# Kernel tuning notes

Hardware: AMD Instinct MI355X
Metric: run time of the kernel (lower is better)

Reference implementation:

```python
import jax, jax.numpy as jnp
import numpy as np

V, D, L, H, T, B = 128, 256, 2, 4, 4096, 8
DK, DV = 128, 256           # key_dim=0.5*D, value_dim=1.0*D (fla GLA defaults)
HK, HV = DK // H, DV // H   # 32, 64
GLN = 16.0                  # gate_logit_normalizer
CH = 64                     # chunk size
EPS = 1e-5

def layernorm(x, w, b):
    mu = x.mean(-1, keepdims=True)
    var = ((x - mu) ** 2).mean(-1, keepdims=True)
    return (x - mu) * jax.lax.rsqrt(var + EPS) * w + b

def gla_chunk(q, k, v, gk, scale):
    # q,k,gk: [B,T,H,HK], v: [B,T,H,HV]; gk are per-key log decay gates (<=0)
    B_, T_, H_, dk = q.shape
    dv = v.shape[-1]
    N = T_ // CH
    def rs(x):
        d = x.shape[-1]
        return x.reshape(B_, N, CH, H_, d).transpose(0, 3, 1, 2, 4)  # [B,H,N,C,d]
    q, k, v, gk = rs(q), rs(k), rs(v), rs(gk)
    b = jnp.cumsum(gk, axis=3)                       # inclusive within-chunk cumlog decay
    q_s = q * jnp.exp(b) * scale
    k_i = k * jnp.exp(-b)                            # for intra-chunk attention
    k_e = k * jnp.exp(b[..., -1:, :] - b)            # decayed to chunk end, for state update
    mask = jnp.tril(jnp.ones((CH, CH), bool))
    att = jnp.einsum('bhncd,bhnmd->bhncm', q_s, k_i)
    att = jnp.where(mask, att, 0.0)
    o_intra = jnp.einsum('bhncm,bhnmd->bhncd', att, v)
    g_last = jnp.exp(b[..., -1, :])                  # [B,H,N,dk] full-chunk decay
    kv = jnp.einsum('bhncd,bhnce->bhnde', k_e, v)    # [B,H,N,dk,dv]
    def step(S, inp):
        qc, gl, kvc = inp
        o = jnp.einsum('bhcd,bhde->bhce', qc, S)
        return S * gl[..., None] + kvc, o
    S0 = jnp.zeros((B_, H_, dk, dv), q.dtype)
    xs = (jnp.moveaxis(q_s, 2, 0), jnp.moveaxis(g_last, 2, 0), jnp.moveaxis(kv, 2, 0))
    _, o_inter = jax.lax.scan(step, S0, xs)
    o = o_intra + jnp.moveaxis(o_inter, 0, 2)        # [B,H,N,C,dv]
    return o.transpose(0, 2, 3, 1, 4).reshape(B_, T_, H_, dv)

def gla_attn(x, wq, wk, wv, wg, gk_w1, gk_w2, gk_b2, gnorm_w, wo):
    B_, T_, _ = x.shape
    q = (x @ wq).reshape(B_, T_, H, HK)
    k = (x @ wk).reshape(B_, T_, H, HK)
    v = (x @ wv).reshape(B_, T_, H, HV)
    gk = jax.nn.log_sigmoid(x @ gk_w1 @ gk_w2 + gk_b2) / GLN
    gk = gk.reshape(B_, T_, H, HK)
    o = gla_chunk(q, k, v, gk, HK ** -0.5)           # [B,T,H,HV]
    g = (x @ wg).reshape(B_, T_, H, HV)
    rms = jax.lax.rsqrt((o * o).mean(-1, keepdims=True) + EPS)
    o = o * rms * gnorm_w * (g * jax.nn.sigmoid(g))  # FusedRMSNormSwishGate
    return o.reshape(B_, T_, DV) @ wo

def setup_inputs() -> dict:
    key = jax.random.key(0)
    ks = jax.random.split(key, 16)
    s = 0.02
    return {
        'tokens': jax.random.randint(ks[0], (B, T), 0, V),
        'embed': jax.random.normal(ks[1], (V, D)) * s,
        'ln_w': jnp.ones((L, D)), 'ln_b': jnp.zeros((L, D)),
        'wq': jax.random.normal(ks[2], (L, D, DK)) * s,
        'wk': jax.random.normal(ks[3], (L, D, DK)) * s,
        'wv': jax.random.normal(ks[4], (L, D, DV)) * s,
        'wg': jax.random.normal(ks[5], (L, D, DV)) * s,
        'gk_w1': jax.random.normal(ks[6], (L, D, 16)) * s,
        'gk_w2': jax.random.normal(ks[7], (L, 16, DK)) * s,
        'gk_b2': jnp.zeros((L, DK)),
        'gnorm_w': jnp.ones((L, HV)),
        'wo': jax.random.normal(ks[8], (L, DV, D)) * s,
        'mlp_w1': jax.random.normal(ks[9], (L, D, 2 * D)) * s,
        'mlp_b1': jnp.zeros((L, 2 * D)),
        'mlp_w2': jax.random.normal(ks[10], (L, 2 * D, D)) * s,
        'mlp_b2': jnp.zeros((L, D)),
        'head_w': jax.random.normal(ks[11], (D, V)) * s,
        'head_b': jnp.zeros((V,)),
    }

def reference(tokens, embed, ln_w, ln_b, wq, wk, wv, wg, gk_w1, gk_w2, gk_b2,
              gnorm_w, wo, mlp_w1, mlp_b1, mlp_w2, mlp_b2, head_w, head_b):
    x = embed[tokens]
    for i in range(L):
        h = layernorm(x, ln_w[i], ln_b[i])
        x = x + gla_attn(h, wq[i], wk[i], wv[i], wg[i], gk_w1[i], gk_w2[i],
                         gk_b2[i], gnorm_w[i], wo[i])
        h = layernorm(x, ln_w[i], ln_b[i])
        x = x + jax.nn.gelu(h @ mlp_w1[i] + mlp_b1[i], approximate=False) @ mlp_w2[i] + mlp_b2[i]
    return x @ head_w + head_b
```

## Files before the change

kernel.cpp:

```cpp
#include <hip/hip_runtime.h>
#include <hip/hip_bf16.h>
#include <math.h>

namespace {

constexpr int Bq = 8, Tq = 4096, Dq = 256, Lq = 2, Hq = 4;
constexpr int DKq = 128, DVq = 256, HKq = 32, HVq = 64;
constexpr int Nq = Tq / 64;
constexpr int Mq = Bq * Tq;
constexpr int SQ = 896;
constexpr float SCALEq = 0.17677669529663688f;
constexpr int WL = 1114112;

typedef __hip_bfloat16 bf16;
typedef __attribute__((ext_vector_type(8))) short bf16x8;
typedef __attribute__((ext_vector_type(4))) float f32x4;

__device__ __forceinline__ float b2f(bf16 x) { return __bfloat162float(x); }

__device__ __forceinline__ bf16x8 ld8(const bf16* p) { return *(const bf16x8*)p; }
__device__ __forceinline__ bf16x8 ld8(const float* p) {
  const float4* q4 = (const float4*)p;
  float4 a = q4[0], b = q4[1];
  float v[8] = {a.x, a.y, a.z, a.w, b.x, b.y, b.z, b.w};
  bf16x8 r;
#pragma unroll
  for (int i = 0; i < 8; i++) r[i] = __builtin_bit_cast(short, __float2bfloat16(v[i]));
  return r;
}

__device__ __forceinline__ void wsplit2(float v, bf16* hi, bf16* lo) {
  bf16 h = __float2bfloat16(v);
  *hi = h; *lo = __float2bfloat16(v - b2f(h));
}

__global__ void k_wprep(const float* __restrict__ wq, const float* __restrict__ wk,
                        const float* __restrict__ wv, const float* __restrict__ wg,
                        const float* __restrict__ g1, const float* __restrict__ g2,
                        const float* __restrict__ wo, const float* __restrict__ m1,
                        const float* __restrict__ m2, const float* __restrict__ hw,
                        bf16* __restrict__ Wt) {
  int g = blockIdx.x * 256 + threadIdx.x;
  if (g >= 2 * 540672 + 32768) return;
  if (g < 2 * 540672) {
    int l = g / 540672, r = g % 540672;
    bf16* dst = Wt + (size_t)l * WL;
    if (r < 196608) {
      int k, nf; float v;
      if (r < 32768)       { int r2 = r;          k = r2 >> 7; nf = (r2 & 127);       v = wq[l*32768 + r2]; }
      else if (r < 65536)  { int r2 = r - 32768;  k = r2 >> 7; nf = 128 + (r2 & 127); v = wk[l*32768 + r2]; }
      else if (r < 131072) { int r2 = r - 65536;  k = r2 >> 8; nf = 256 + (r2 & 255); v = wv[l*65536 + r2]; }
      else                 { int r2 = r - 131072; k = r2 >> 8; nf = 512 + (r2 & 255); v = wg[l*65536 + r2]; }
      wsplit2(v, &dst[(size_t)nf*256 + k], &dst[229376 + (size_t)nf*256 + k]);
    } else if (r < 212992) {
      int r2 = r - 196608; int k = r2 >> 7, n = r2 & 127;
      float v = 0.f;
#pragma unroll
      for (int i = 0; i < 16; i++) v += g1[l*4096 + k*16 + i] * g2[l*2048 + i*128 + n];
      int nf = 768 + n;
      wsplit2(v, &dst[(size_t)nf*256 + k], &dst[229376 + (size_t)nf*256 + k]);
    } else if (r < 278528) {
      int r2 = r - 212992; int k = r2 >> 8, n = r2 & 255;
      wsplit2(wo[l*65536 + r2], &dst[458752 + (size_t)n*256 + k], &dst[524288 + (size_t)n*256 + k]);
    } else if (r < 409600) {
      int r2 = r - 278528; int k = r2 >> 9, n = r2 & 511;
      wsplit2(m1[l*131072 + r2], &dst[589824 + (size_t)n*256 + k], &dst[720896 + (size_t)n*256 + k]);
    } else {
      int r2 = r - 409600; int k = r2 >> 8, n = r2 & 255;
      wsplit2(m2[l*131072 + r2], &dst[851968 + (size_t)n*512 + k], &dst[983040 + (size_t)n*512 + k]);
    }
  } else {
    int r2 = g - 2 * 540672; int k = r2 >> 7, n = r2 & 127;
    wsplit2(hw[r2], &Wt[2228224 + (size_t)n*256 + k], &Wt[2228224 + 32768 + (size_t)n*256 + k]);
  }
}

__global__ void k_embed(const int* __restrict__ tok, const float* __restrict__ emb,
                        float* __restrict__ x) {
  int row = blockIdx.x, i = threadIdx.x;
  x[(size_t)row * Dq + i] = emb[(size_t)tok[row] * Dq + i];
}

__global__ void k_ln(const float* __restrict__ x, const float* __restrict__ w,
                     const float* __restrict__ bb, bf16* __restrict__ h) {
  int row = blockIdx.x, i = threadIdx.x;
  float v = x[(size_t)row * Dq + i];
  float s = v, s2 = v * v;
#pragma unroll
  for (int o = 32; o > 0; o >>= 1) { s += __shfl_down(s, o, 64); s2 += __shfl_down(s2, o, 64); }
  __shared__ float rs[4], rs2[4];
  if ((i & 63) == 0) { rs[i >> 6] = s; rs2[i >> 6] = s2; }
  __syncthreads();
  float sum = rs[0] + rs[1] + rs[2] + rs[3];
  float sum2 = rs2[0] + rs2[1] + rs2[2] + rs2[3];
  float mu = sum * (1.f / Dq);
  float var = fmaxf(sum2 * (1.f / Dq) - mu * mu, 0.f);
  float r = rsqrtf(var + 1e-5f);
  h[(size_t)row * Dq + i] = __float2bfloat16((v - mu) * r * w[i] + bb[i]);
}

template <typename AT, typename OT, int EPI, bool BIAS, bool ACC>
__global__ __launch_bounds__(256) void k_mgemm(const AT* __restrict__ A,
                                               const bf16* __restrict__ Wt,
                                               const float* __restrict__ bias,
                                               OT* __restrict__ C, int K, int N) {
  __shared__ __attribute__((aligned(16))) bf16 At[128 * 72];
  __shared__ __attribute__((aligned(16))) bf16 Bh[128 * 72];
  __shared__ __attribute__((aligned(16))) bf16 Bl[128 * 72];
  const bf16* Whi = Wt;
  const bf16* Wlo = Wt + (size_t)K * N;
  int tid = threadIdx.x;
  int row0 = blockIdx.x * 128, col0 = blockIdx.y * 128;
  int lane = tid & 63, wave = tid >> 6;
  int wm = (wave >> 1) * 64, wn = (wave & 1) * 64;
  int lr = lane & 15, lk = (lane >> 4) * 8;
  f32x4 acc[4][4];
#pragma unroll
  for (int m = 0; m < 4; m++)
#pragma unroll
    for (int n = 0; n < 4; n++) acc[m][n] = (f32x4){0.f, 0.f, 0.f, 0.f};

  for (int k0 = 0; k0 < K; k0 += 64) {
#pragma unroll
    for (int p = 0; p < 4; p++) {
      int cix = p * 256 + tid, r = cix >> 3, j = (cix & 7) * 8;
      *(bf16x8*)&At[r * 72 + j] = ld8(A + (size_t)(row0 + r) * K + k0 + j);
    }
#pragma unroll
    for (int p = 0; p < 4; p++) {
      int cix = p * 256 + tid, r = cix >> 3, j = (cix & 7) * 8;
      size_t go = (size_t)(col0 + r) * K + k0 + j;
      *(bf16x8*)&Bh[r * 72 + j] = *(const bf16x8*)(Whi + go);
      *(bf16x8*)&Bl[r * 72 + j] = *(const bf16x8*)(Wlo + go);
    }
    __syncthreads();
#pragma unroll
    for (int kk = 0; kk < 64; kk += 32) {
      bf16x8 af[4], bhf[4], blf[4];
#pragma unroll
      for (int m = 0; m < 4; m++) af[m] = *(bf16x8*)&At[(wm + m * 16 + lr) * 72 + kk + lk];
#pragma unroll
      for (int n = 0; n < 4; n++) {
        bhf[n] = *(bf16x8*)&Bh[(wn + n * 16 + lr) * 72 + kk + lk];
        blf[n] = *(bf16x8*)&Bl[(wn + n * 16 + lr) * 72 + kk + lk];
      }
#pragma unroll
      for (int m = 0; m < 4; m++)
#pragma unroll
        for (int n = 0; n < 4; n++) {
          acc[m][n] = __builtin_amdgcn_mfma_f32_16x16x32_bf16(af[m], bhf[n], acc[m][n], 0, 0, 0);
          acc[m][n] = __builtin_amdgcn_mfma_f32_16x16x32_bf16(af[m], blf[n], acc[m][n], 0, 0, 0);
        }
    }
    __syncthreads();
  }
#pragma unroll
  for (int m = 0; m < 4; m++) {
#pragma unroll
    for (int n = 0; n < 4; n++) {
      int col = col0 + wn + n * 16 + lr;
      int rowb = row0 + wm + m * 16 + (lane >> 4) * 4;
      float bv = BIAS ? bias[col] : 0.f;
#pragma unroll
      for (int j = 0; j < 4; j++) {
        float v = acc[m][n][j] + bv;
        if (EPI == 2) v = 0.5f * v * (1.f + erff(v * 0.70710678118654752f));
        if (EPI == 3 && col >= 768) {
          float t = v + bias[col - 768];
          v = (fminf(t, 0.f) - log1pf(expf(-fabsf(t)))) * (1.f / 16.f);
        }
        size_t oi = (size_t)(rowb + j) * N + col;
        if constexpr (ACC) C[oi] += v;
        else if constexpr (sizeof(OT) == 2) C[oi] = __float2bfloat16(v);
        else C[oi] = v;
      }
    }
  }
}

__global__ __launch_bounds__(256) void k_intra(bf16* QKVG,
                                               bf16* __restrict__ O,
                                               bf16* __restrict__ KVt,
                                               float* __restrict__ GL) {
  int blk = blockIdx.x;
  int n = blk & 63, h = (blk >> 6) & 3, b = blk >> 8;
  __shared__ __attribute__((aligned(16))) char smem[47488];
  float* bshT = (float*)smem;
  bf16*  kvS  = (bf16*)smem;
  float* glv  = (float*)(smem + 8448);
  bf16*  vT   = (bf16*)(smem + 8576);
  bf16*  kiAH = (bf16*)(smem + 17792);
  bf16*  kiAL = (bf16*)(smem + 22400);
  bf16*  qsH  = (bf16*)(smem + 27008);
  bf16*  qsL  = (bf16*)(smem + 32128);
  bf16*  kiBH = (bf16*)(smem + 37248);
  bf16*  kiBL = (bf16*)(smem + 42368);
  bf16*  aH   = (bf16*)(smem + 27008);
  bf16*  aL   = (bf16*)(smem + 36224);
  int tid = threadIdx.x;
  int lane = tid & 63, wave = tid >> 6;
  int lr = lane & 15, lg = lane >> 4;
  size_t tbase = (size_t)b * Tq + n * 64;
  int bh = b * Hq + h;

  {
    int c = tid >> 2, dc = (tid & 3) * 8;
    bf16x8 g8 = *(const bf16x8*)(QKVG + (tbase + c) * SQ + 768 + h * HKq + dc);
#pragma unroll
    for (int i = 0; i < 8; i++) bshT[(dc + i) * 66 + c] = b2f(__builtin_bit_cast(bf16, (short)g8[i]));
  }
  __syncthreads();
#pragma unroll
  for (int dd = 0; dd < 8; dd++) {
    int d = wave * 8 + dd;
    float v = bshT[d * 66 + lane];
#pragma unroll
    for (int o = 1; o < 64; o <<= 1) {
      float t = __shfl_up(v, (unsigned)o, 64);
      if (lane >= o) v += t;
    }
    bshT[d * 66 + lane] = v;
  }
  __syncthreads();
  if (tid < 32) {
    float g = expf(bshT[tid * 66 + 63]);
    glv[tid] = g;
    GL[(size_t)(bh * Nq + n) * 32 + tid] = g;
  }
  {
    int c = tid >> 2, dc = (tid & 3) * 8;
    size_t qoff = (tbase + c) * SQ + h * HKq + dc;
    bf16x8 q8 = *(const bf16x8*)(QKVG + qoff);
    bf16x8 k8 = *(const bf16x8*)(QKVG + qoff + 128);
    bf16x8 qh8, ql8, kh8, kl8;
#pragma unroll
    for (int i = 0; i < 8; i++) {
      float bv = bshT[(dc + i) * 66 + c];
      float qv = b2f(__builtin_bit_cast(bf16, (short)q8[i])) * expf(bv) * SCALEq;
      float kv = b2f(__builtin_bit_cast(bf16, (short)k8[i])) * expf(-bv);
      bf16 qh = __float2bfloat16(qv); bf16 ql = __float2bfloat16(qv - b2f(qh));
      bf16 kh = __float2bfloat16(kv); bf16 kl = __float2bfloat16(kv - b2f(kh));
      qh8[i] = __builtin_bit_cast(short, qh); ql8[i] = __builtin_bit_cast(short, ql);
      kh8[i] = __builtin_bit_cast(short, kh); kl8[i] = __builtin_bit_cast(short, kl);
      kiAH[(dc + i) * 72 + c] = kh; kiAL[(dc + i) * 72 + c] = kl;
    }
    *(bf16x8*)&qsH[c * 40 + dc] = qh8;
    *(bf16x8*)&qsL[c * 40 + dc] = ql8;
    *(bf16x8*)&kiBH[c * 40 + dc] = kh8;
    *(bf16x8*)&kiBL[c * 40 + dc] = kl8;
    *(bf16x8*)(QKVG + qoff) = qh8;
  }
#pragma unroll
  for (int p = 0; p < 2; p++) {
    int idx = p * 256 + tid;
    int c = idx & 63, ec = (idx >> 6) * 8;
    bf16x8 v8 = *(const bf16x8*)(QKVG + (tbase + c) * SQ + 256 + h * HVq + ec);
#pragma unroll
    for (int i = 0; i < 8; i++) vT[(ec + i) * 72 + c] = __builtin_bit_cast(bf16, (short)v8[i]);
  }
  __syncthreads();
  f32x4 accq[4];
#pragma unroll
  for (int t = 0; t < 4; t++) accq[t] = (f32x4){0.f, 0.f, 0.f, 0.f};
  {
    bf16x8 afh = *(bf16x8*)&qsH[(wave * 16 + lr) * 40 + lg * 8];
    bf16x8 afl = *(bf16x8*)&qsL[(wave * 16 + lr) * 40 + lg * 8];
#pragma unroll
    for (int t = 0; t < 4; t++) {
      bf16x8 bh = *(bf16x8*)&kiBH[(t * 16 + lr) * 40 + lg * 8];
      bf16x8 bl = *(bf16x8*)&kiBL[(t * 16 + lr) * 40 + lg * 8];
      accq[t] = __builtin_amdgcn_mfma_f32_16x16x32_bf16(afh, bh, accq[t], 0, 0, 0);
      accq[t] = __builtin_amdgcn_mfma_f32_16x16x32_bf16(afh, bl, accq[t], 0, 0, 0);
      accq[t] = __builtin_amdgcn_mfma_f32_16x16x32_bf16(afl, bh, accq[t], 0, 0, 0);
    }
  }
  __syncthreads();
#pragma unroll
  for (int t = 0; t < 4; t++)
#pragma unroll
    for (int j = 0; j < 4; j++) {
      int row = wave * 16 + lg * 4 + j;
      int col = t * 16 + lr;
      float v = (col <= row) ? accq[t][j] : 0.f;
      bf16 hi = __float2bfloat16(v);
      aH[row * 72 + col] = hi;
      aL[row * 72 + col] = __float2bfloat16(v - b2f(hi));
    }
  __syncthreads();
  f32x4 acco[4];
#pragma unroll
  for (int t = 0; t < 4; t++) acco[t] = (f32x4){0.f, 0.f, 0.f, 0.f};
#pragma unroll
  for (int ks = 0; ks < 2; ks++) {
    bf16x8 ah = *(bf16x8*)&aH[(wave * 16 + lr) * 72 + ks * 32 + lg * 8];
    bf16x8 al = *(bf16x8*)&aL[(wave * 16 + lr) * 72 + ks * 32 + lg * 8];
#pragma unroll
    for (int t = 0; t < 4; t++) {
      bf16x8 bfv = *(bf16x8*)&vT[(t * 16 + lr) * 72 + ks * 32 + lg * 8];
      acco[t] = __builtin_amdgcn_mfma_f32_16x16x32_bf16(ah, bfv, acco[t], 0, 0, 0);
      acco[t] = __builtin_amdgcn_mfma_f32_16x16x32_bf16(al, bfv, acco[t], 0, 0, 0);
    }
  }
#pragma unroll
  for (int t = 0; t < 4; t++)
#pragma unroll
    for (int j = 0; j < 4; j++) {
      int row = wave * 16 + lg * 4 + j, e = t * 16 + lr;
      O[(tbase + row) * DVq + h * HVq + e] = __float2bfloat16(acco[t][j]);
    }
  f32x4 acck[2];
  acck[0] = (f32x4){0.f, 0.f, 0.f, 0.f};
  acck[1] = (f32x4){0.f, 0.f, 0.f, 0.f};
#pragma unroll
  for (int ks = 0; ks < 2; ks++) {
    bf16x8 akh = *(bf16x8*)&kiAH[((wave >> 1) * 16 + lr) * 72 + ks * 32 + lg * 8];
    bf16x8 akl = *(bf16x8*)&kiAL[((wave >> 1) * 16 + lr) * 72 + ks * 32 + lg * 8];
#pragma unroll
    for (int t = 0; t < 2; t++) {
      bf16x8 bfv = *(bf16x8*)&vT[(((wave & 1) * 2 + t) * 16 + lr) * 72 + ks * 32 + lg * 8];
      acck[t] = __builtin_amdgcn_mfma_f32_16x16x32_bf16(akh, bfv, acck[t], 0, 0, 0);
      acck[t] = __builtin_amdgcn_mfma_f32_16x16x32_bf16(akl, bfv, acck[t], 0, 0, 0);
    }
  }
#pragma unroll
  for (int t = 0; t < 2; t++)
#pragma unroll
    for (int j = 0; j < 4; j++) {
      int d = (wave >> 1) * 16 + lg * 4 + j;
      int e = ((wave & 1) * 2 + t) * 16 + lr;
      kvS[d * 72 + e] = __float2bfloat16(acck[t][j] * glv[d]);
    }
  __syncthreads();
  size_t kbase = (size_t)(bh * Nq + n) * 2048;
  {
    int d = tid >> 3, cc = (tid & 7) * 8;
    *(bf16x8*)&KVt[kbase + d * 64 + cc] = *(bf16x8*)&kvS[d * 72 + cc];
  }
}

__global__ __launch_bounds__(256) void k_inter(const bf16* __restrict__ QKVG,
                                               const float* __restrict__ GL,
                                               const bf16* __restrict__ KVt,
                                               bf16* __restrict__ O) {
  int blk = blockIdx.x;
  int es = blk & 7, h = (blk >> 3) & 3, b = blk >> 5;
  int e0 = es * 8;
  __shared__ __attribute__((aligned(16))) bf16 kvl[64 * 32 * 8];
  __shared__ float gl[64 * 32];
  __shared__ float S[64 * 32 * 8];
  int tid = threadIdx.x;
  int bh = b * Hq + h;
  const float* glp = GL + (size_t)bh * Nq * 32;
#pragma unroll
  for (int p = 0; p < 8; p++) { int i = p * 256 + tid; gl[i] = glp[i]; }
  const bf16* kvp = KVt + (size_t)bh * Nq * 2048 + e0;
#pragma unroll
  for (int p = 0; p < 8; p++) {
    int c8 = p * 256 + tid;
    *(bf16x8*)&kvl[c8 * 8] = *(const bf16x8*)(kvp + (size_t)(c8 >> 5) * 2048 + (size_t)(c8 & 31) * 64);
  }
  __syncthreads();
  {
    int pe = tid & 7, pd = tid >> 3;
    float s = 0.f;
    for (int n = 0; n < 64; n++) {
      S[(n * 32 + pd) * 8 + pe] = s;
      s = s * gl[n * 32 + pd] + b2f(kvl[(n * 32 + pd) * 8 + pe]);
    }
  }
  __syncthreads();
  int c = tid >> 2, ep = tid & 3;
  for (int n = 0; n < 64; n++) {
    size_t tbase = (size_t)b * Tq + n * 64;
    const bf16* qp = QKVG + (tbase + c) * SQ + h * HKq;
    const float* Sp = &S[n * 256];
    float a0 = 0.f, a1 = 0.f;
#pragma unroll
    for (int j = 0; j < 4; j++) {
      bf16x8 q8 = *(const bf16x8*)(qp + j * 8);
#pragma unroll
      for (int i = 0; i < 8; i++) {
        float qf = b2f(__builtin_bit_cast(bf16, (short)q8[i]));
        int d = j * 8 + i;
        a0 += qf * Sp[d * 8 + ep];
        a1 += qf * Sp[d * 8 + ep + 4];
      }
    }
    size_t oi = (tbase + c) * DVq + h * HVq + e0 + ep;
    O[oi] = __float2bfloat16(b2f(O[oi]) + a0);
    O[oi + 4] = __float2bfloat16(b2f(O[oi + 4]) + a1);
  }
}

__global__ void k_gate(bf16* __restrict__ O, const bf16* __restrict__ QKVG,
                       const float* __restrict__ gnw) {
  int row = blockIdx.x, tid = threadIdx.x;
  int e = tid & 63;
  float o = b2f(O[(size_t)row * DVq + tid]);
  float s = o * o;
#pragma unroll
  for (int of = 32; of > 0; of >>= 1) s += __shfl_xor(s, of, 64);
  float r = rsqrtf(s * (1.f / 64.f) + 1e-5f);
  float g = b2f(QKVG[(size_t)row * SQ + 512 + tid]);
  float sw = g / (1.f + expf(-g));
  O[(size_t)row * DVq + tid] = __float2bfloat16(o * r * gnw[e] * sw);
}

}

extern "C" void kernel_launch(void* const* d_in, const int* in_sizes, int n_in,
                              void* d_out, int out_size, void* d_ws, size_t ws_size,
                              hipStream_t stream) {
  const int*   tok  = (const int*)d_in[0];
  const float* emb  = (const float*)d_in[1];
  const float* ln_w = (const float*)d_in[2];
  const float* ln_b = (const float*)d_in[3];
  const float* wq   = (const float*)d_in[4];
  const float* wk   = (const float*)d_in[5];
  const float* wv   = (const float*)d_in[6];
  const float* wg   = (const float*)d_in[7];
  const float* gkw1 = (const float*)d_in[8];
  const float* gkw2 = (const float*)d_in[9];
  const float* gkb2 = (const float*)d_in[10];
  const float* gnw  = (const float*)d_in[11];
  const float* wo   = (const float*)d_in[12];
  const float* mw1  = (const float*)d_in[13];
  const float* mb1  = (const float*)d_in[14];
  const float* mw2  = (const float*)d_in[15];
  const float* mb2  = (const float*)d_in[16];
  const float* hw   = (const float*)d_in[17];
  const float* hb   = (const float*)d_in[18];

  if (ws_size < 134217728u) return;
  char* w = (char*)d_ws;
  float* X    = (float*)w;
  bf16*  Ob   = (bf16*)(w + 33554432);
  bf16*  Hbf  = Ob;
  bf16*  QKVG = (bf16*)(w + 50331648);
  bf16*  KVt  = (bf16*)(w + 109051904);
  float* GLb  = (float*)(w + 117440512);
  bf16*  Wt   = (bf16*)(w + 117702656);
  bf16*  MLPH = QKVG;

  dim3 blk(256);
  k_wprep<<<4353, blk, 0, stream>>>(wq, wk, wv, wg, gkw1, gkw2, wo, mw1, mw2, hw, Wt);
  k_embed<<<Mq, blk, 0, stream>>>(tok, emb, X);

  for (int l = 0; l < Lq; l++) {
    const bf16* Wl = Wt + (size_t)l * WL;
    k_ln<<<Mq, blk, 0, stream>>>(X, ln_w + l * Dq, ln_b + l * Dq, Hbf);
    k_mgemm<bf16, bf16, 3, false, false><<<dim3(256, 7), blk, 0, stream>>>(Hbf, Wl, gkb2 + l * DKq, QKVG, 256, SQ);
    k_intra<<<Bq * Hq * Nq, blk, 0, stream>>>(QKVG, Ob, KVt, GLb);
    k_inter<<<Bq * Hq * 8, blk, 0, stream>>>(QKVG, GLb, KVt, Ob);
    k_gate<<<Mq, blk, 0, stream>>>(Ob, QKVG, gnw + l * HVq);
    k_mgemm<bf16, float, 0, false, true><<<dim3(256, 2), blk, 0, stream>>>(Ob, Wl + 458752, nullptr, X, 256, 256);
    k_ln<<<Mq, blk, 0, stream>>>(X, ln_w + l * Dq, ln_b + l * Dq, Hbf);
    k_mgemm<bf16, bf16, 2, true, false><<<dim3(256, 4), blk, 0, stream>>>(Hbf, Wl + 589824, mb1 + l * 2 * Dq, MLPH, 256, 512);
    k_mgemm<bf16, float, 0, true, true><<<dim3(256, 2), blk, 0, stream>>>(MLPH, Wl + 851968, mb2 + l * Dq, X, 512, 256);
  }
  k_mgemm<float, float, 0, true, false><<<dim3(256, 1), blk, 0, stream>>>(X, Wt + 2228224, hb, (float*)d_out, 256, 128);
}
```

Baseline: 698.3 us.

## Keep full-K A tile resident in LDS and stream swizzled weights via global_load_lds

The GEMM kernel now loads the whole 128x256 activation tile into LDS once per block and loops over all output column tiles, so the activation is read from global memory only once rather than once per column tile. Weight tiles are brought in with double-buffered direct global-to-LDS loads, and all prepacked weights use an XOR swizzle to avoid LDS bank conflicts. The K=512 MLP down projection is split into two accumulating launches. Each launch now uses only 256 blocks with larger LDS usage, which lowers parallelism and occupancy, and the extra launch adds another read-modify-write of X.

New measurement: 868.1 us. +24.3%, slower.

```diff
diff --git a/kernel.cpp b/kernel.cpp
--- a/kernel.cpp
+++ b/kernel.cpp
@@ -27,6 +27,15 @@
 #pragma unroll
   for (int i = 0; i < 8; i++) r[i] = __builtin_bit_cast(short, __float2bfloat16(v[i]));
   return r;
+}
+
+__device__ __forceinline__ void gl_lds16(const void* g, void* l) {
+  __builtin_amdgcn_global_load_lds((const __attribute__((address_space(1))) void*)g,
+                                   (__attribute__((address_space(3))) void*)l, 16, 0, 0);
+}
+
+__device__ __forceinline__ int swzk(int k, int row) {
+  return (k & ~63) | ((((k >> 3) & 7) ^ (row & 7)) << 3) | (k & 7);
 }
 
 __device__ __forceinline__ void wsplit2(float v, bf16* hi, bf16* lo) {
@@ -51,27 +60,33 @@
       else if (r < 65536)  { int r2 = r - 32768;  k = r2 >> 7; nf = 128 + (r2 & 127); v = wk[l*32768 + r2]; }
       else if (r < 131072) { int r2 = r - 65536;  k = r2 >> 8; nf = 256 + (r2 & 255); v = wv[l*65536 + r2]; }
       else                 { int r2 = r - 131072; k = r2 >> 8; nf = 512 + (r2 & 255); v = wg[l*65536 + r2]; }
-      wsplit2(v, &dst[(size_t)nf*256 + k], &dst[229376 + (size_t)nf*256 + k]);
+      int ks = swzk(k, nf);
+      wsplit2(v, &dst[(size_t)nf*256 + ks], &dst[229376 + (size_t)nf*256 + ks]);
     } else if (r < 212992) {
       int r2 = r - 196608; int k = r2 >> 7, n = r2 & 127;
       float v = 0.f;
 #pragma unroll
       for (int i = 0; i < 16; i++) v += g1[l*4096 + k*16 + i] * g2[l*2048 + i*128 + n];
       int nf = 768 + n;
-      wsplit2(v, &dst[(size_t)nf*256 + k], &dst[229376 + (size_t)nf*256 + k]);
+      int ks = swzk(k, nf);
+      wsplit2(v, &dst[(size_t)nf*256 + ks], &dst[229376 + (size_t)nf*256 + ks]);
     } else if (r < 278528) {
       int r2 = r - 212992; int k = r2 >> 8, n = r2 & 255;
-      wsplit2(wo[l*65536 + r2], &dst[458752 + (size_t)n*256 + k], &dst[524288 + (size_t)n*256 + k]);
+      int ks = swzk(k, n);
+      wsplit2(wo[l*65536 + r2], &dst[458752 + (size_t)n*256 + ks], &dst[524288 + (size_t)n*256 + ks]);
     } else if (r < 409600) {
       int r2 = r - 278528; int k = r2 >> 9, n = r2 & 511;
-      wsplit2(m1[l*131072 + r2], &dst[589824 + (size_t)n*256 + k], &dst[720896 + (size_t)n*256 + k]);
+      int ks = swzk(k, n);
+      wsplit2(m1[l*131072 + r2], &dst[589824 + (size_t)n*256 + ks], &dst[720896 + (size_t)n*256 + ks]);
     } else {
       int r2 = r - 409600; int k = r2 >> 8, n = r2 & 255;
-      wsplit2(m2[l*131072 + r2], &dst[851968 + (size_t)n*512 + k], &dst[983040 + (size_t)n*512 + k]);
+      int ks = swzk(k, n);
+      wsplit2(m2[l*131072 + r2], &dst[851968 + (size_t)n*512 + ks], &dst[983040 + (size_t)n*512 + ks]);
     }
   } else {
     int r2 = g - 2 * 540672; int k = r2 >> 7, n = r2 & 127;
-    wsplit2(hw[r2], &Wt[2228224 + (size_t)n*256 + k], &Wt[2228224 + 32768 + (size_t)n*256 + k]);
+    int ks = swzk(k, n);
+    wsplit2(hw[r2], &Wt[2228224 + (size_t)n*256 + ks], &Wt[2228224 + 32768 + (size_t)n*256 + ks]);
   }
 }
 
@@ -100,81 +115,113 @@
 }
 
 template <typename AT, typename OT, int EPI, bool BIAS, bool ACC>
-__global__ __launch_bounds__(256) void k_mgemm(const AT* __restrict__ A,
-                                               const bf16* __restrict__ Wt,
-                                               const float* __restrict__ bias,
-                                               OT* __restrict__ C, int K, int N) {
-  __shared__ __attribute__((aligned(16))) bf16 At[128 * 72];
-  __shared__ __attribute__((aligned(16))) bf16 Bh[128 * 72];
-  __shared__ __attribute__((aligned(16))) bf16 Bl[128 * 72];
-  const bf16* Whi = Wt;
-  const bf16* Wlo = Wt + (size_t)K * N;
+__global__ __launch_bounds__(256) void k_mgemm3(const AT* __restrict__ A, int lda,
+                                                const bf16* __restrict__ Wh,
+                                                const bf16* __restrict__ Wl, int ldw,
+                                                const float* __restrict__ bias,
+                                                OT* __restrict__ C, int ldc, int N) {
+  __shared__ __attribute__((aligned(16))) bf16 At[128 * 256];
+  __shared__ __attribute__((aligned(16))) bf16 BH[2][8192];
+  __shared__ __attribute__((aligned(16))) bf16 BL[2][8192];
   int tid = threadIdx.x;
-  int row0 = blockIdx.x * 128, col0 = blockIdx.y * 128;
   int lane = tid & 63, wave = tid >> 6;
+  int lr = lane & 15, lg = lane >> 4;
   int wm = (wave >> 1) * 64, wn = (wave & 1) * 64;
-  int lr = lane & 15, lk = (lane >> 4) * 8;
+  int row0 = blockIdx.x * 128;
+  int nty = N >> 7, ncell = nty * 4;
+
+  auto ISSUE = [&](int cell, int buf) {
+    int y = cell >> 2, k = cell & 3, col0 = y * 128;
+#pragma unroll
+    for (int i = 0; i < 4; i++) {
+      int r = col0 + i * 32 + wave * 8 + (lane >> 3);
+      int c = k * 64 + (lane & 7) * 8;
+      int lo = i * 2048 + wave * 512;
+      gl_lds16(Wh + (size_t)r * ldw + c, &BH[buf][lo]);
+      gl_lds16(Wl + (size_t)r * ldw + c, &BL[buf][lo]);
+    }
+  };
+
+  ISSUE(0, 0);
+#pragma unroll
+  for (int p = 0; p < 16; p++) {
+    int g = p * 256 + tid;
+    int r = g >> 5, c8 = (g & 31) * 8;
+    bf16x8 v = ld8(A + (size_t)(row0 + r) * lda + c8);
+    *(bf16x8*)&At[r * 256 + swzk(c8, r)] = v;
+  }
+  asm volatile("s_waitcnt lgkmcnt(0)" ::: "memory");
+  __builtin_amdgcn_sched_barrier(0);
+  __builtin_amdgcn_s_barrier();
+
   f32x4 acc[4][4];
 #pragma unroll
   for (int m = 0; m < 4; m++)
 #pragma unroll
     for (int n = 0; n < 4; n++) acc[m][n] = (f32x4){0.f, 0.f, 0.f, 0.f};
 
-  for (int k0 = 0; k0 < K; k0 += 64) {
-#pragma unroll
-    for (int p = 0; p < 4; p++) {
-      int cix = p * 256 + tid, r = cix >> 3, j = (cix & 7) * 8;
-      *(bf16x8*)&At[r * 72 + j] = ld8(A + (size_t)(row0 + r) * K + k0 + j);
-    }
-#pragma unroll
-    for (int p = 0; p < 4; p++) {
-      int cix = p * 256 + tid, r = cix >> 3, j = (cix & 7) * 8;
-      size_t go = (size_t)(col0 + r) * K + k0 + j;
-      *(bf16x8*)&Bh[r * 72 + j] = *(const bf16x8*)(Whi + go);
-      *(bf16x8*)&Bl[r * 72 + j] = *(const bf16x8*)(Wlo + go);
-    }
-    __syncthreads();
+  for (int cell = 0; cell < ncell; cell++) {
+    int buf = cell & 1;
+    if (cell + 1 < ncell) {
+      ISSUE(cell + 1, buf ^ 1);
+      asm volatile("s_waitcnt vmcnt(8)" ::: "memory");
+    } else {
+      asm volatile("s_waitcnt vmcnt(0)" ::: "memory");
+    }
+    __builtin_amdgcn_sched_barrier(0);
+    __builtin_amdgcn_s_barrier();
+    int k = cell & 3;
 #pragma unroll
     for (int kk = 0; kk < 64; kk += 32) {
-      bf16x8 af[4], bhf[4], blf[4];
-#pragma unroll
-      for (int m = 0; m < 4; m++) af[m] = *(bf16x8*)&At[(wm + m * 16 + lr) * 72 + kk + lk];
+      bf16x8 af[4], bh4[4], bl4[4];
+#pragma unroll
+      for (int m = 0; m < 4; m++) {
+        int ar = wm + m * 16 + lr;
+        int ka = k * 64 + kk + lg * 8;
+        af[m] = *(bf16x8*)&At[ar * 256 + swzk(ka, ar)];
+      }
 #pragma unroll
       for (int n = 0; n < 4; n++) {
-        bhf[n] = *(bf16x8*)&Bh[(wn + n * 16 + lr) * 72 + kk + lk];
-        blf[n] = *(bf16x8*)&Bl[(wn + n * 16 + lr) * 72 + kk + lk];
+        int br = wn + n * 16 + lr;
+        int cs = (((kk + lg * 8) >> 3) ^ (br & 7)) << 3;
+        bh4[n] = *(bf16x8*)&BH[buf][br * 64 + cs];
+        bl4[n] = *(bf16x8*)&BL[buf][br * 64 + cs];
       }
 #pragma unroll
       for (int m = 0; m < 4; m++)
 #pragma unroll
         for (int n = 0; n < 4; n++) {
-          acc[m][n] = __builtin_amdgcn_mfma_f32_16x16x32_bf16(af[m], bhf[n], acc[m][n], 0, 0, 0);
-          acc[m][n] = __builtin_amdgcn_mfma_f32_16x16x32_bf16(af[m], blf[n], acc[m][n], 0, 0, 0);
+          acc[m][n] = __builtin_amdgcn_mfma_f32_16x16x32_bf16(af[m], bh4[n], acc[m][n], 0, 0, 0);
+          acc[m][n] = __builtin_amdgcn_mfma_f32_16x16x32_bf16(af[m], bl4[n], acc[m][n], 0, 0, 0);
         }
     }
-    __syncthreads();
-  }
-#pragma unroll
-  for (int m = 0; m < 4; m++) {
-#pragma unroll
-    for (int n = 0; n < 4; n++) {
-      int col = col0 + wn + n * 16 + lr;
-      int rowb = row0 + wm + m * 16 + (lane >> 4) * 4;
-      float bv = BIAS ? bias[col] : 0.f;
-#pragma unroll
-      for (int j = 0; j < 4; j++) {
-        float v = acc[m][n][j] + bv;
-        if (EPI == 2) v = 0.5f * v * (1.f + erff(v * 0.70710678118654752f));
-        if (EPI == 3 && col >= 768) {
-          float t = v + bias[col - 768];
-          v = (fminf(t, 0.f) - log1pf(expf(-fabsf(t)))) * (1.f / 16.f);
+    if (k == 3) {
+      int col0 = (cell >> 2) * 128;
+#pragma unroll
+      for (int m = 0; m < 4; m++) {
+#pragma unroll
+        for (int n = 0; n < 4; n++) {
+          int col = col0 + wn + n * 16 + lr;
+          int rowb = row0 + wm + m * 16 + lg * 4;
+          float bv = BIAS ? bias[col] : 0.f;
+#pragma unroll
+          for (int j = 0; j < 4; j++) {
+            float v = acc[m][n][j] + bv;
+            if (EPI == 2) v = 0.5f * v * (1.f + erff(v * 0.70710678118654752f));
+            if (EPI == 3 && col >= 768) {
+              float t = v + bias[col - 768];
+              v = (fminf(t, 0.f) - log1pf(expf(-fabsf(t)))) * (1.f / 16.f);
+            }
+            size_t oi = (size_t)(rowb + j) * ldc + col;
+            if constexpr (ACC) C[oi] += v;
+            else if constexpr (sizeof(OT) == 2) C[oi] = __float2bfloat16(v);
+            else C[oi] = v;
+          }
+          acc[m][n] = (f32x4){0.f, 0.f, 0.f, 0.f};
         }
-        size_t oi = (size_t)(rowb + j) * N + col;
-        if constexpr (ACC) C[oi] += v;
-        else if constexpr (sizeof(OT) == 2) C[oi] = __float2bfloat16(v);
-        else C[oi] = v;
       }
     }
+    __builtin_amdgcn_s_barrier();
   }
 }
 
@@ -449,14 +496,15 @@
   for (int l = 0; l < Lq; l++) {
     const bf16* Wl = Wt + (size_t)l * WL;
     k_ln<<<Mq, blk, 0, stream>>>(X, ln_w + l * Dq, ln_b + l * Dq, Hbf);
-    k_mgemm<bf16, bf16, 3, false, false><<<dim3(256, 7), blk, 0, stream>>>(Hbf, Wl, gkb2 + l * DKq, QKVG, 256, SQ);
+    k_mgemm3<bf16, bf16, 3, false, false><<<256, blk, 0, stream>>>(Hbf, 256, Wl, Wl + 229376, 256, gkb2 + l * DKq, QKVG, SQ, SQ);
     k_intra<<<Bq * Hq * Nq, blk, 0, stream>>>(QKVG, Ob, KVt, GLb);
     k_inter<<<Bq * Hq * 8, blk, 0, stream>>>(QKVG, GLb, KVt, Ob);
     k_gate<<<Mq, blk, 0, stream>>>(Ob, QKVG, gnw + l * HVq);
-    k_mgemm<bf16, float, 0, false, true><<<dim3(256, 2), blk, 0, stream>>>(Ob, Wl + 458752, nullptr, X, 256, 256);
+    k_mgemm3<bf16, float, 0, false, true><<<256, blk, 0, stream>>>(Ob, 256, Wl + 458752, Wl + 524288, 256, nullptr, X, 256, 256);
     k_ln<<<Mq, blk, 0, stream>>>(X, ln_w + l * Dq, ln_b + l * Dq, Hbf);
-    k_mgemm<bf16, bf16, 2, true, false><<<dim3(256, 4), blk, 0, stream>>>(Hbf, Wl + 589824, mb1 + l * 2 * Dq, MLPH, 256, 512);
-    k_mgemm<bf16, float, 0, true, true><<<dim3(256, 2), blk, 0, stream>>>(MLPH, Wl + 851968, mb2 + l * Dq, X, 512, 256);
-  }
-  k_mgemm<float, float, 0, true, false><<<dim3(256, 1), blk, 0, stream>>>(X, Wt + 2228224, hb, (float*)d_out, 256, 128);
-}
+    k_mgemm3<bf16, bf16, 2, true, false><<<256, blk, 0, stream>>>(Hbf, 256, Wl + 589824, Wl + 720896, 256, mb1 + l * 2 * Dq, MLPH, 512, 512);
+    k_mgemm3<bf16, float, 0, true, true><<<256, blk, 0, stream>>>(MLPH, 512, Wl + 851968, Wl + 983040, 512, mb2 + l * Dq, X, 256, 256);
+    k_mgemm3<bf16, float, 0, false, true><<<256, blk, 0, stream>>>(MLPH + 256, 512, Wl + 851968 + 256, Wl + 983040 + 256, 512, nullptr, X, 256, 256);
+  }
+  k_mgemm3<float, float, 0, true, false><<<256, blk, 0, stream>>>(X, 256, Wt + 2228224, Wt + 2228224 + 32768, 256, hb, (float*)d_out, 128, 128);
+}
```
